# Optimization experiments

Measured on AMD Instinct MI355X. Metric: run time of the kernel, lower is better.

The kernel has to match this reference:

```python
import jax, jax.numpy as jnp
import numpy as np

NT, NC = 100000, 25000
ETT, ECT = 800000, 400000
DIN_T, DIN_C = 64, 32
H, C = 4, 32
HID = H * C  # 128
SLOPE = 0.2  # GATConv LeakyReLU negative slope


def setup_inputs() -> dict:
    key = jax.random.key(0)
    ks = jax.random.split(key, 24)
    def p(i, shape, s=0.05):
        return jax.random.normal(ks[i], shape, dtype=jnp.float32) * s
    return {
        'x_target': jax.random.normal(ks[0], (NT, DIN_T), dtype=jnp.float32),
        'x_context': jax.random.normal(ks[1], (NC, DIN_C), dtype=jnp.float32),
        'edge_tt': jax.random.randint(ks[2], (2, ETT), 0, NT),
        'edge_ct_src': jax.random.randint(ks[3], (ECT,), 0, NC),
        'edge_ct_dst': jax.random.randint(ks[4], (ECT,), 0, NT),
        'W_pre_t': p(5, (DIN_T, HID)), 'b_pre_t': jnp.zeros((HID,), jnp.float32),
        'W_pre_c': p(6, (DIN_C, HID)), 'b_pre_c': jnp.zeros((HID,), jnp.float32),
        'W_sd': p(7, (HID, HID)), 'att_src_sd': p(8, (H, C)), 'att_dst_sd': p(9, (H, C)), 'b_sd': jnp.zeros((HID,), jnp.float32),
        'W_ds': p(10, (HID, HID)), 'att_src_ds': p(11, (H, C)), 'att_dst_ds': p(12, (H, C)), 'b_ds': jnp.zeros((HID,), jnp.float32),
        'W_ct_src': p(13, (HID, HID)), 'W_ct_dst': p(14, (HID, HID)), 'att_src_ct': p(15, (H, C)), 'att_dst_ct': p(16, (H, C)), 'b_ct': jnp.zeros((HID,), jnp.float32),
        'W_out': p(17, (HID, HID)), 'b_out': jnp.zeros((HID,), jnp.float32),
    }


def _gat(h_src, h_dst, att_s, att_d, src, dst, n_dst, bias):
    # h_src: [N_src,H,C] transformed src feats; h_dst: [N_dst,H,C]
    a_s = jnp.einsum('nhc,hc->nh', h_src, att_s)  # [N_src,H]
    a_d = jnp.einsum('nhc,hc->nh', h_dst, att_d)  # [N_dst,H]
    e = a_s[src] + a_d[dst]                        # [E,H]
    e = jnp.where(e > 0, e, SLOPE * e)             # LeakyReLU(0.2)
    m = jax.ops.segment_max(e, dst, num_segments=n_dst)  # stable softmax per dst
    ex = jnp.exp(e - m[dst])
    den = jax.ops.segment_sum(ex, dst, num_segments=n_dst)
    alpha = ex / den[dst]                          # [E,H]
    msg = h_src[src] * alpha[:, :, None]           # [E,H,C]
    out = jax.ops.segment_sum(msg, dst, num_segments=n_dst)
    return out.reshape(n_dst, H * C) + bias


def reference(x_target, x_context, edge_tt, edge_ct_src, edge_ct_dst,
              W_pre_t, b_pre_t, W_pre_c, b_pre_c,
              W_sd, att_src_sd, att_dst_sd, b_sd,
              W_ds, att_src_ds, att_dst_ds, b_ds,
              W_ct_src, W_ct_dst, att_src_ct, att_dst_ct, b_ct,
              W_out, b_out):
    # HeteroDictLinear pretransform + relu
    h_t = jax.nn.relu(x_target @ W_pre_t + b_pre_t)   # [NT,128]
    h_c = jax.nn.relu(x_context @ W_pre_c + b_pre_c)  # [NC,128]
    res = h_t
    # DirGATConv on (target,to,target): forward + reversed, each w/ self-loops
    loops = jnp.arange(NT)
    src_f = jnp.concatenate([edge_tt[0], loops]); dst_f = jnp.concatenate([edge_tt[1], loops])
    src_r = jnp.concatenate([edge_tt[1], loops]); dst_r = jnp.concatenate([edge_tt[0], loops])
    hs = (h_t @ W_sd).reshape(NT, H, C)
    out_sd = _gat(hs, hs, att_src_sd, att_dst_sd, src_f, dst_f, NT, b_sd)
    hd = (h_t @ W_ds).reshape(NT, H, C)
    out_ds = _gat(hd, hd, att_src_ds, att_dst_ds, src_r, dst_r, NT, b_ds)
    out_tt = 0.5 * out_sd + 0.5 * out_ds  # (1-alpha), alpha with alpha=0.5
    # bipartite GATConv on (context,to,target), no self loops
    hcs = (h_c @ W_ct_src).reshape(NC, H, C)
    htd = (h_t @ W_ct_dst).reshape(NT, H, C)
    out_ct = _gat(hcs, htd, att_src_ct, att_dst_ct, edge_ct_src, edge_ct_dst, NT, b_ct)
    # HeteroConv aggr='mean' over the two edge types hitting 'target'
    x = 0.5 * (out_tt + out_ct)
    x = jax.nn.relu(x + res)  # skip connection + relu
    return x @ W_out + b_out
```

## Files before the change

kernel.cpp:

```cpp
#include <hip/hip_runtime.h>
#include <cstdint>
#include <cstddef>

typedef unsigned short u16;
typedef unsigned int u32;

#define NT 100000
#define NC 25000
#define ETT 800000
#define ECT 400000
#define SLOPE 0.2f
#define LOG2E 1.4426950408889634f
#define OFFS (NT + 4)

#define NBK 782
#define NBLK 256
#define CHT ((ETT + NBLK - 1) / NBLK)
#define CHC ((ECT + NBLK - 1) / NBLK)
#define TOTC (3 * NBK * NBLK)
#define NSB ((TOTC + 2047) / 2048)

typedef __attribute__((ext_vector_type(8))) short bf16x8;
typedef __attribute__((ext_vector_type(4))) float f32x4;

__device__ __forceinline__ u16 f2bf(float f) {
  u32 u = __float_as_uint(f);
  u32 r = (u >> 16) & 1u;
  return (u16)((u + 0x7fffu + r) >> 16);
}
__device__ __forceinline__ float lof(u32 p) { return __uint_as_float(p << 16); }
__device__ __forceinline__ float hif(u32 p) { return __uint_as_float(p & 0xffff0000u); }

#define GT_BLK ((NT + 31) / 32)
#define GC_BLK ((NC + 31) / 32)

__global__ __launch_bounds__(256) void transform_kernel(
    const float* __restrict__ Wsd, const float* __restrict__ AsSd, const float* __restrict__ AdSd,
    const float* __restrict__ Wds, const float* __restrict__ AsDs, const float* __restrict__ AdDs,
    const float* __restrict__ Wout,
    u16* __restrict__ bf_sd, u16* __restrict__ bf_ds, u16* __restrict__ bf_out,
    const float* __restrict__ Wcd, const float* __restrict__ attD,
    const float* __restrict__ bsd, const float* __restrict__ bds, const float* __restrict__ bct,
    float* __restrict__ cbias,
    const float* __restrict__ x_t, const float* __restrict__ Wpt, const float* __restrict__ bpt,
    u16* __restrict__ h_t, float* __restrict__ aD,
    const float* __restrict__ x_c, const float* __restrict__ Wpc, const float* __restrict__ bpc,
    const float* __restrict__ Wcs, const float* __restrict__ attS,
    u16* __restrict__ hc_bf, float* __restrict__ aS_c)
{
  __shared__ float s_a[32][33];
  __shared__ float s_b[32][128];
  __shared__ float s_c[32][132];
  const int b = blockIdx.x;
  const int t = threadIdx.x;

  if (b < 4) {
    if (b == 3) {
      if (t < 128) cbias[t] = 0.25f * bsd[t] + 0.25f * bds[t] + 0.5f * bct[t];
      return;
    }
    float* fS = &s_c[0][0];
    float* fD = fS + 512;
    const float* W = (b == 0) ? Wsd : (b == 1) ? Wds : Wout;
    const float* As = (b == 0) ? AsSd : AsDs;
    const float* Ad = (b == 0) ? AdSd : AdDs;
    u16* out = (b == 0) ? bf_sd : (b == 1) ? bf_ds : bf_out;
    const int tiles = (b == 2) ? 8 : 9;
    if (b < 2) {
      if (t < 128) {
        for (int h = 0; h < 4; ++h) {
          float s1 = 0.f, s2 = 0.f;
          for (int c = 0; c < 32; ++c) {
            const float wv = W[t * 128 + h * 32 + c];
            s1 = fmaf(wv, As[h * 32 + c], s1);
            s2 = fmaf(wv, Ad[h * 32 + c], s2);
          }
          fS[t * 4 + h] = s1 * LOG2E; fD[t * 4 + h] = s2 * LOG2E;
        }
      }
      __syncthreads();
    }
    const int total = tiles * 4 * 64 * 8;
    for (int i = t; i < total; i += 256) {
      const int j = i & 7, lane = (i >> 3) & 63, ks = (i >> 9) & 3, ti = i >> 11;
      const int k = ks * 32 + (lane >> 4) * 8 + j;
      const int n = ti * 16 + (lane & 15);
      float v;
      if (n < 128) v = W[k * 128 + n];
      else if (n < 132) v = fS[k * 4 + (n - 128)];
      else if (n < 136) v = fD[k * 4 + (n - 132)];
      else v = 0.f;
      out[i] = f2bf(v);
    }
    return;
  }

  if (b < 4 + GT_BLK) {
    float* s_fold = &s_c[0][0];
    if (t < 128) {
      for (int h = 0; h < 4; ++h) {
        float s = 0.f;
        for (int c = 0; c < 32; ++c)
          s = fmaf(Wcd[t * 128 + h * 32 + c], attD[h * 32 + c], s);
        s_fold[t * 4 + h] = s * LOG2E;
      }
    }
    const int row0 = (b - 4) * 32;
    const int rl = t >> 3, cg = t & 7;
    const int gr = row0 + rl;
    float acc[4][4];
    for (int g = 0; g < 4; ++g)
      for (int j = 0; j < 4; ++j)
        acc[g][j] = bpt[g * 32 + cg * 4 + j];
    for (int kc = 0; kc < 64; kc += 32) {
      {
        float4 f = make_float4(0.f, 0.f, 0.f, 0.f);
        if (gr < NT) f = *(const float4*)(x_t + (size_t)gr * 64 + kc + cg * 4);
        s_a[rl][cg * 4 + 0] = f.x; s_a[rl][cg * 4 + 1] = f.y;
        s_a[rl][cg * 4 + 2] = f.z; s_a[rl][cg * 4 + 3] = f.w;
      }
      for (int j = 0; j < 4; ++j) {
        const int idx = t + j * 256;
        const int k = idx >> 5, c4 = (idx & 31) * 4;
        *(float4*)&s_b[k][c4] = *(const float4*)(Wpt + (size_t)(kc + k) * 128 + c4);
      }
      __syncthreads();
#pragma unroll 8
      for (int k = 0; k < 32; ++k) {
        const float a = s_a[rl][k];
        for (int g = 0; g < 4; ++g) {
          const float4 w = *(const float4*)&s_b[k][g * 32 + cg * 4];
          acc[g][0] = fmaf(a, w.x, acc[g][0]);
          acc[g][1] = fmaf(a, w.y, acc[g][1]);
          acc[g][2] = fmaf(a, w.z, acc[g][2]);
          acc[g][3] = fmaf(a, w.w, acc[g][3]);
        }
      }
      __syncthreads();
    }
    if (gr < NT) {
      float p0 = 0.f, p1 = 0.f, p2 = 0.f, p3 = 0.f;
      for (int g = 0; g < 4; ++g) {
        for (int j = 0; j < 4; ++j) acc[g][j] = fmaxf(acc[g][j], 0.f);
        uint2 pk;
        pk.x = (u32)f2bf(acc[g][0]) | ((u32)f2bf(acc[g][1]) << 16);
        pk.y = (u32)f2bf(acc[g][2]) | ((u32)f2bf(acc[g][3]) << 16);
        *(uint2*)(h_t + (size_t)gr * 128 + g * 32 + cg * 4) = pk;
        for (int j = 0; j < 4; ++j) {
          const int col = g * 32 + cg * 4 + j;
          const float4 f4 = *(const float4*)&s_fold[col * 4];
          const float a = acc[g][j];
          p0 = fmaf(a, f4.x, p0); p1 = fmaf(a, f4.y, p1);
          p2 = fmaf(a, f4.z, p2); p3 = fmaf(a, f4.w, p3);
        }
      }
      for (int m = 1; m < 8; m <<= 1) {
        p0 += __shfl_xor(p0, m); p1 += __shfl_xor(p1, m);
        p2 += __shfl_xor(p2, m); p3 += __shfl_xor(p3, m);
      }
      if (cg == 0) *(float4*)(aD + (size_t)gr * 4) = make_float4(p0, p1, p2, p3);
    }
    return;
  }

  {
    const int row0 = (b - 4 - GT_BLK) * 32;
    const int rl = t >> 3, cg = t & 7;
    const int gr = row0 + rl;
    {
      float4 f = make_float4(0.f, 0.f, 0.f, 0.f);
      if (gr < NC) f = *(const float4*)(x_c + (size_t)gr * 32 + cg * 4);
      s_a[rl][cg * 4 + 0] = f.x; s_a[rl][cg * 4 + 1] = f.y;
      s_a[rl][cg * 4 + 2] = f.z; s_a[rl][cg * 4 + 3] = f.w;
    }
    for (int j = 0; j < 4; ++j) {
      const int idx = t + j * 256;
      const int k = idx >> 5, c4 = (idx & 31) * 4;
      *(float4*)&s_b[k][c4] = *(const float4*)(Wpc + (size_t)k * 128 + c4);
    }
    __syncthreads();
    float acc[4][4];
    for (int g = 0; g < 4; ++g)
      for (int j = 0; j < 4; ++j) acc[g][j] = bpc[g * 32 + cg * 4 + j];
#pragma unroll 8
    for (int k = 0; k < 32; ++k) {
      const float a = s_a[rl][k];
      for (int g = 0; g < 4; ++g) {
        const float4 w = *(const float4*)&s_b[k][g * 32 + cg * 4];
        acc[g][0] = fmaf(a, w.x, acc[g][0]);
        acc[g][1] = fmaf(a, w.y, acc[g][1]);
        acc[g][2] = fmaf(a, w.z, acc[g][2]);
        acc[g][3] = fmaf(a, w.w, acc[g][3]);
      }
    }
    for (int g = 0; g < 4; ++g)
      *(float4*)&s_c[rl][g * 32 + cg * 4] =
          make_float4(fmaxf(acc[g][0], 0.f), fmaxf(acc[g][1], 0.f),
                      fmaxf(acc[g][2], 0.f), fmaxf(acc[g][3], 0.f));
    __syncthreads();
    float acc2[4][4];
    for (int g = 0; g < 4; ++g)
      for (int j = 0; j < 4; ++j) acc2[g][j] = 0.f;
    for (int kc = 0; kc < 128; kc += 32) {
      for (int j = 0; j < 4; ++j) {
        const int idx = t + j * 256;
        const int k = idx >> 5, c4 = (idx & 31) * 4;
        *(float4*)&s_b[k][c4] = *(const float4*)(Wcs + (size_t)(kc + k) * 128 + c4);
      }
      __syncthreads();
#pragma unroll 8
      for (int k = 0; k < 32; ++k) {
        const float a = s_c[rl][kc + k];
        for (int g = 0; g < 4; ++g) {
          const float4 w = *(const float4*)&s_b[k][g * 32 + cg * 4];
          acc2[g][0] = fmaf(a, w.x, acc2[g][0]);
          acc2[g][1] = fmaf(a, w.y, acc2[g][1]);
          acc2[g][2] = fmaf(a, w.z, acc2[g][2]);
          acc2[g][3] = fmaf(a, w.w, acc2[g][3]);
        }
      }
      __syncthreads();
    }
    if (gr < NC) {
      float pS[4];
      for (int g = 0; g < 4; ++g) {
        uint2 pk;
        pk.x = (u32)f2bf(acc2[g][0]) | ((u32)f2bf(acc2[g][1]) << 16);
        pk.y = (u32)f2bf(acc2[g][2]) | ((u32)f2bf(acc2[g][3]) << 16);
        *(uint2*)(hc_bf + (size_t)gr * 128 + g * 32 + cg * 4) = pk;
        const float4 as4 = *(const float4*)(attS + g * 32 + cg * 4);
        pS[g] = acc2[g][0] * as4.x + acc2[g][1] * as4.y + acc2[g][2] * as4.z + acc2[g][3] * as4.w;
      }
      for (int m = 1; m < 8; m <<= 1)
        for (int g = 0; g < 4; ++g) pS[g] += __shfl_xor(pS[g], m);
      if (cg == 0)
        *(float4*)(aS_c + (size_t)gr * 4) =
            make_float4(pS[0] * LOG2E, pS[1] * LOG2E, pS[2] * LOG2E, pS[3] * LOG2E);
    }
  }
}

__global__ __launch_bounds__(256) void mfma_logits2_kernel(
    const short* __restrict__ A, const short* __restrict__ Bsd, const short* __restrict__ Bds,
    u16* __restrict__ hs, float* __restrict__ aSsd, float* __restrict__ aDsd,
    u16* __restrict__ hd, float* __restrict__ aSds, float* __restrict__ aDds, int M)
{
  __shared__ __align__(16) float lds[4][16][148];
  const int wv = threadIdx.x >> 6, lane = threadIdx.x & 63;
  const int quad = lane >> 4, l16 = lane & 15;
  const int row0 = blockIdx.x * 64 + wv * 16;
  const int arow = min(row0 + l16, M - 1);
  const short* ap = A + (size_t)arow * 128 + quad * 8;
  bf16x8 af[4];
  for (int ks = 0; ks < 4; ++ks) af[ks] = *(const bf16x8*)(ap + ks * 32);
  const int row = row0 + l16;
  const int idx = lane & 7, rr = lane >> 3;
  for (int pass = 0; pass < 2; ++pass) {
    const short* B = pass ? Bds : Bsd;
    u16* outb = pass ? hd : hs;
    float* aS = pass ? aSds : aSsd;
    float* aD = pass ? aDds : aDsd;
    f32x4 acc[9];
    for (int t = 0; t < 9; ++t) acc[t] = (f32x4){0.f, 0.f, 0.f, 0.f};
    for (int ks = 0; ks < 4; ++ks)
      for (int t = 0; t < 9; ++t) {
        const bf16x8 bf = *(const bf16x8*)(B + ((t * 4 + ks) * 64 + lane) * 8);
        acc[t] = __builtin_amdgcn_mfma_f32_16x16x32_bf16(af[ks], bf, acc[t], 0, 0, 0);
      }
    for (int t = 0; t < 9; ++t)
      for (int r = 0; r < 4; ++r)
        lds[wv][quad * 4 + r][t * 16 + l16] = acc[t][r];
    __syncthreads();
    if (row < M) {
      for (int g = 0; g < 8; ++g) {
        const f32x4 v = *(const f32x4*)&lds[wv][l16][g * 16 + quad * 4];
        uint2 pk;
        pk.x = (u32)f2bf(v[0]) | ((u32)f2bf(v[1]) << 16);
        pk.y = (u32)f2bf(v[2]) | ((u32)f2bf(v[3]) << 16);
        *(uint2*)(outb + (size_t)row * 128 + g * 16 + quad * 4) = pk;
      }
    }
    for (int p = 0; p < 2; ++p) {
      const int lr = p * 8 + rr;
      const int n = row0 + lr;
      if (n < M) {
        const float v = lds[wv][lr][128 + idx];
        if (idx < 4) aS[(size_t)n * 4 + idx] = v;
        else aD[(size_t)n * 4 + idx - 4] = v;
      }
    }
    __syncthreads();
  }
}

__global__ __launch_bounds__(256) void mfma_out_kernel(
    const short* __restrict__ A, const short* __restrict__ B,
    const float* __restrict__ bias, float* __restrict__ out, int M)
{
  __shared__ __align__(16) float lds[4][16][132];
  const int wv = threadIdx.x >> 6, lane = threadIdx.x & 63;
  const int quad = lane >> 4, l16 = lane & 15;
  const int row0 = blockIdx.x * 64 + wv * 16;
  const int arow = min(row0 + l16, M - 1);
  const short* ap = A + (size_t)arow * 128 + quad * 8;
  bf16x8 af[4];
  for (int ks = 0; ks < 4; ++ks) af[ks] = *(const bf16x8*)(ap + ks * 32);
  f32x4 acc[8];
  for (int t = 0; t < 8; ++t) acc[t] = (f32x4){0.f, 0.f, 0.f, 0.f};
  for (int ks = 0; ks < 4; ++ks)
    for (int t = 0; t < 8; ++t) {
      const bf16x8 bf = *(const bf16x8*)(B + ((t * 4 + ks) * 64 + lane) * 8);
      acc[t] = __builtin_amdgcn_mfma_f32_16x16x32_bf16(af[ks], bf, acc[t], 0, 0, 0);
    }
  for (int t = 0; t < 8; ++t)
    for (int r = 0; r < 4; ++r)
      lds[wv][quad * 4 + r][t * 16 + l16] = acc[t][r];
  __syncthreads();
  const int row = row0 + l16;
  if (row < M) {
    for (int g = 0; g < 8; ++g) {
      const int col = g * 16 + quad * 4;
      f32x4 v = *(const f32x4*)&lds[wv][l16][col];
      const f32x4 b4 = *(const f32x4*)(bias + col);
      v = v + b4;
      *(f32x4*)(out + (size_t)row * 128 + col) = v;
    }
  }
}

__global__ __launch_bounds__(256) void hist_blk_kernel(const int* __restrict__ tt_src,
    const int* __restrict__ tt_dst, const int* __restrict__ ect_d, int* __restrict__ cntblk)
{
  __shared__ int h[3 * NBK];
  const int t = threadIdx.x, b = blockIdx.x;
  for (int i = t; i < 3 * NBK; i += 256) h[i] = 0;
  __syncthreads();
  const int lo = b * CHT, hi = min(lo + CHT, ETT);
  for (int i = lo + t; i < hi; i += 256) {
    atomicAdd(&h[tt_dst[i] >> 7], 1);
    atomicAdd(&h[NBK + (tt_src[i] >> 7)], 1);
  }
  const int lo2 = b * CHC, hi2 = min(lo2 + CHC, ECT);
  for (int i = lo2 + t; i < hi2; i += 256)
    atomicAdd(&h[2 * NBK + (ect_d[i] >> 7)], 1);
  __syncthreads();
  for (int i = t; i < 3 * NBK; i += 256)
    cntblk[(size_t)i * NBLK + b] = h[i];
}

__global__ __launch_bounds__(256) void scan2_blk_kernel(const int* __restrict__ in,
    int* __restrict__ out, int* __restrict__ bsum)
{
  const int t = threadIdx.x, b = blockIdx.x;
  const int idx = b * 2048 + t * 8;
  int v[8];
  int s = 0;
  if (idx < TOTC) {
    const int4 q0 = *(const int4*)(in + idx);
    const int4 q1 = *(const int4*)(in + idx + 4);
    int x;
    x = q0.x; v[0] = s; s += x;  x = q0.y; v[1] = s; s += x;
    x = q0.z; v[2] = s; s += x;  x = q0.w; v[3] = s; s += x;
    x = q1.x; v[4] = s; s += x;  x = q1.y; v[5] = s; s += x;
    x = q1.z; v[6] = s; s += x;  x = q1.w; v[7] = s; s += x;
  } else {
    for (int j = 0; j < 8; ++j) v[j] = 0;
  }
  __shared__ int sh[256];
  sh[t] = s;
  __syncthreads();
  for (int d = 1; d < 256; d <<= 1) {
    const int u = (t >= d) ? sh[t - d] : 0;
    __syncthreads();
    sh[t] += u;
    __syncthreads();
  }
  const int excl = (t == 0) ? 0 : sh[t - 1];
  if (idx < TOTC) {
    int4 q0, q1;
    q0.x = excl + v[0]; q0.y = excl + v[1]; q0.z = excl + v[2]; q0.w = excl + v[3];
    q1.x = excl + v[4]; q1.y = excl + v[5]; q1.z = excl + v[6]; q1.w = excl + v[7];
    *(int4*)(out + idx) = q0;
    *(int4*)(out + idx + 4) = q1;
  }
  if (t == 255) bsum[b] = sh[255];
}

__global__ __launch_bounds__(512) void scan2_top_kernel(const int* __restrict__ bsum,
    int* __restrict__ bpre)
{
  __shared__ int sh[512];
  const int t = threadIdx.x;
  const int orig = (t < NSB) ? bsum[t] : 0;
  sh[t] = orig;
  __syncthreads();
  for (int d = 1; d < 512; d <<= 1) {
    const int v = (t >= d) ? sh[t - d] : 0;
    __syncthreads();
    sh[t] += v;
    __syncthreads();
  }
  if (t < NSB) bpre[t] = sh[t] - orig;
}

__global__ __launch_bounds__(256) void bin_kernel(const int* __restrict__ tt_src,
    const int* __restrict__ tt_dst, const int* __restrict__ ect_s, const int* __restrict__ ect_d,
    const int* __restrict__ scanned, const int* __restrict__ bpre, u32* __restrict__ bin)
{
  __shared__ int cur[3 * NBK];
  const int t = threadIdx.x, b = blockIdx.x;
  for (int i = t; i < 3 * NBK; i += 256) {
    const int idx = i * NBLK + b;
    cur[i] = scanned[idx] + bpre[idx >> 11];
  }
  __syncthreads();
  const int lo = b * CHT, hi = min(lo + CHT, ETT);
  for (int i = lo + t; i < hi; i += 256) {
    const int s = tt_src[i], d = tt_dst[i];
    int p = atomicAdd(&cur[d >> 7], 1);
    bin[p] = ((u32)(d & 127) << 17) | (u32)s;
    p = atomicAdd(&cur[NBK + (s >> 7)], 1);
    bin[p] = ((u32)(s & 127) << 17) | (u32)d;
  }
  const int lo2 = b * CHC, hi2 = min(lo2 + CHC, ECT);
  for (int i = lo2 + t; i < hi2; i += 256) {
    const int s = ect_s[i], d = ect_d[i];
    const int p = atomicAdd(&cur[2 * NBK + (d >> 7)], 1);
    bin[p] = ((u32)(d & 127) << 17) | (u32)s;
  }
}

__global__ __launch_bounds__(256) void bucket_fill_kernel(const int* __restrict__ scanned,
    const int* __restrict__ bpre, const u32* __restrict__ bin,
    int* __restrict__ offs, int* __restrict__ big_el)
{
  const int rel = blockIdx.x / NBK;
  const int bucket = blockIdx.x - rel * NBK;
  const int t = threadIdx.x;
  __shared__ int s_cnt[128], s_exc[128], s_cur[128];
  if (t < 128) s_cnt[t] = 0;
  __syncthreads();
  const int bi = blockIdx.x * NBLK;
  const int base = scanned[bi] + bpre[bi >> 11];
  const int nxt = (blockIdx.x == 3 * NBK - 1) ? (2 * ETT + ECT)
                                              : scanned[bi + NBLK] + bpre[(bi + NBLK) >> 11];
  const int size = nxt - base;
  for (int i = t; i < size; i += 256)
    atomicAdd(&s_cnt[bin[base + i] >> 17], 1);
  __syncthreads();
  if (t < 128) s_exc[t] = s_cnt[t];
  __syncthreads();
  for (int d = 1; d < 128; d <<= 1) {
    int v = 0;
    if (t < 128 && t >= d) v = s_exc[t - d];
    __syncthreads();
    if (t < 128) s_exc[t] += v;
    __syncthreads();
  }
  const int relbase = rel * ETT;
  const int obase = base - relbase;
  int* off_rel = offs + (size_t)rel * OFFS;
  const int node0 = bucket * 128;
  if (t < 128) {
    const int excl = s_exc[t] - s_cnt[t];
    s_cur[t] = obase + excl;
    if (node0 + t < NT) off_rel[node0 + t] = obase + excl;
  }
  if (t == 0 && bucket == NBK - 1) off_rel[NT] = obase + size;
  __syncthreads();
  int* el_rel = big_el + relbase;
  for (int i = t; i < size; i += 256) {
    const u32 e = bin[base + i];
    const int pos = atomicAdd(&s_cur[e >> 17], 1);
    el_rel[pos] = (int)(e & 0x1FFFFu);
  }
}

__device__ __forceinline__ void gat_pipe16(const int* __restrict__ off,
    const int* __restrict__ el, const float* __restrict__ aS, const float* __restrict__ aD,
    const u16* __restrict__ hb, int d, int h, int cb, int self_loop, float w,
    float* __restrict__ acc)
{
  const float ad = aD[(size_t)d * 4 + h];
  const int beg = off[d];
  const int m = off[d + 1] - beg;
  const int cnt = m + self_loop;
  if (cnt <= 0) return;
  float den = 0.f;
  float a0 = 0.f, a1 = 0.f, a2 = 0.f, a3 = 0.f, a4 = 0.f, a5 = 0.f, a6 = 0.f, a7 = 0.f;
  int sB = (1 < m) ? el[beg + 1] : d;
  {
    const int sA0 = (0 < m) ? el[beg] : d;
    float eA = aS[(size_t)sA0 * 4 + h];
    uint4 pA = *(const uint4*)(hb + (size_t)sA0 * 128 + cb);
    for (int k = 0; k < cnt; ++k) {
      const int sC = (k + 2 < m) ? el[beg + k + 2] : d;
      const float eB = aS[(size_t)sB * 4 + h];
      const uint4 pB = *(const uint4*)(hb + (size_t)sB * 128 + cb);
      float ea = eA + ad;
      ea = ea > 0.f ? ea : SLOPE * ea;
      const float ex = exp2f(ea);
      den += ex;
      a0 = fmaf(ex, lof(pA.x), a0); a1 = fmaf(ex, hif(pA.x), a1);
      a2 = fmaf(ex, lof(pA.y), a2); a3 = fmaf(ex, hif(pA.y), a3);
      a4 = fmaf(ex, lof(pA.z), a4); a5 = fmaf(ex, hif(pA.z), a5);
      a6 = fmaf(ex, lof(pA.w), a6); a7 = fmaf(ex, hif(pA.w), a7);
      eA = eB; pA = pB; sB = sC;
    }
  }
  const float s = w / den;
  acc[0] = fmaf(a0, s, acc[0]); acc[1] = fmaf(a1, s, acc[1]);
  acc[2] = fmaf(a2, s, acc[2]); acc[3] = fmaf(a3, s, acc[3]);
  acc[4] = fmaf(a4, s, acc[4]); acc[5] = fmaf(a5, s, acc[5]);
  acc[6] = fmaf(a6, s, acc[6]); acc[7] = fmaf(a7, s, acc[7]);
}

__global__ __launch_bounds__(256) void gather_all_kernel(
    const int* __restrict__ off_f, const int* __restrict__ el_f,
    const float* __restrict__ aS_sd, const float* __restrict__ aD_sd, const u16* __restrict__ hs,
    const int* __restrict__ off_r, const int* __restrict__ el_r,
    const float* __restrict__ aS_ds, const float* __restrict__ aD_ds, const u16* __restrict__ hd,
    const int* __restrict__ off_c, const int* __restrict__ el_c,
    const float* __restrict__ aS_ct, const float* __restrict__ aD_ct, const u16* __restrict__ hc,
    const u16* __restrict__ skip, const float* __restrict__ cbias, u16* __restrict__ x)
{
  const int d = blockIdx.x * 16 + (threadIdx.x >> 4);
  if (d >= NT) return;
  const int lg = threadIdx.x & 15;
  const int h = lg >> 2;
  const int cb = lg * 8;
  float acc[8];
  for (int i = 0; i < 8; ++i) acc[i] = 0.f;
  gat_pipe16(off_f, el_f, aS_sd, aD_sd, hs, d, h, cb, 1, 0.25f, acc);
  gat_pipe16(off_r, el_r, aS_ds, aD_ds, hd, d, h, cb, 1, 0.25f, acc);
  gat_pipe16(off_c, el_c, aS_ct, aD_ct, hc, d, h, cb, 0, 0.5f, acc);
  const uint4 sk = *(const uint4*)(skip + (size_t)d * 128 + cb);
  const float4 cb0 = *(const float4*)(cbias + cb);
  const float4 cb1 = *(const float4*)(cbias + cb + 4);
  const float o0 = fmaxf(acc[0] + cb0.x + lof(sk.x), 0.f);
  const float o1 = fmaxf(acc[1] + cb0.y + hif(sk.x), 0.f);
  const float o2 = fmaxf(acc[2] + cb0.z + lof(sk.y), 0.f);
  const float o3 = fmaxf(acc[3] + cb0.w + hif(sk.y), 0.f);
  const float o4 = fmaxf(acc[4] + cb1.x + lof(sk.z), 0.f);
  const float o5 = fmaxf(acc[5] + cb1.y + hif(sk.z), 0.f);
  const float o6 = fmaxf(acc[6] + cb1.z + lof(sk.w), 0.f);
  const float o7 = fmaxf(acc[7] + cb1.w + hif(sk.w), 0.f);
  uint4 r;
  r.x = (u32)f2bf(o0) | ((u32)f2bf(o1) << 16);
  r.y = (u32)f2bf(o2) | ((u32)f2bf(o3) << 16);
  r.z = (u32)f2bf(o4) | ((u32)f2bf(o5) << 16);
  r.w = (u32)f2bf(o6) | ((u32)f2bf(o7) << 16);
  *(uint4*)(x + (size_t)d * 128 + cb) = r;
}

extern "C" void kernel_launch(void* const* d_in, const int* in_sizes, int n_in,
                              void* d_out, int out_size, void* d_ws, size_t ws_size,
                              hipStream_t stream)
{
  const float* x_t   = (const float*)d_in[0];
  const float* x_c   = (const float*)d_in[1];
  const int*   e_tt  = (const int*)d_in[2];
  const int*   ect_s = (const int*)d_in[3];
  const int*   ect_d = (const int*)d_in[4];
  const float* Wpt = (const float*)d_in[5];   const float* bpt = (const float*)d_in[6];
  const float* Wpc = (const float*)d_in[7];   const float* bpc = (const float*)d_in[8];
  const float* Wsd = (const float*)d_in[9];   const float* As_sd = (const float*)d_in[10];
  const float* Ad_sd = (const float*)d_in[11]; const float* bsd = (const float*)d_in[12];
  const float* Wds = (const float*)d_in[13];  const float* As_ds = (const float*)d_in[14];
  const float* Ad_ds = (const float*)d_in[15]; const float* bds = (const float*)d_in[16];
  const float* Wcs = (const float*)d_in[17];  const float* Wcd = (const float*)d_in[18];
  const float* As_ct = (const float*)d_in[19]; const float* Ad_ct = (const float*)d_in[20];
  const float* bct = (const float*)d_in[21];
  const float* Wout = (const float*)d_in[22]; const float* bout = (const float*)d_in[23];

  char* p = (char*)d_ws;
  size_t off = 0;
  auto alloc = [&](size_t bytes) { char* r = p + off; off += (bytes + 255) & ~(size_t)255; return r; };
  u16* ht_bf   = (u16*)alloc((size_t)NT * 128 * 2);
  u16* hs_bf   = (u16*)alloc((size_t)NT * 128 * 2);
  u16* hd_bf   = (u16*)alloc((size_t)NT * 128 * 2);
  u16* hc_bf   = (u16*)alloc((size_t)NC * 128 * 2);
  u16* x_bf    = (u16*)alloc((size_t)NT * 128 * 2);
  float* aS_sd = (float*)alloc((size_t)NT * 4 * 4);
  float* aD_sd = (float*)alloc((size_t)NT * 4 * 4);
  float* aS_ds = (float*)alloc((size_t)NT * 4 * 4);
  float* aD_ds = (float*)alloc((size_t)NT * 4 * 4);
  float* aS_ct = (float*)alloc((size_t)NC * 4 * 4);
  float* aD_ct = (float*)alloc((size_t)NT * 4 * 4);
  int* cntblk  = (int*)alloc((size_t)TOTC * 4);
  int* scanned = (int*)alloc((size_t)TOTC * 4);
  u32* bin     = (u32*)alloc((size_t)(2 * ETT + ECT) * 4);
  int* big_el  = (int*)alloc((size_t)(2 * ETT + ECT) * 4);
  int* offs    = (int*)alloc((size_t)3 * OFFS * 4);
  int* bsum    = (int*)alloc((size_t)NSB * 4);
  int* bpre    = (int*)alloc((size_t)NSB * 4);
  float* cbias   = (float*)alloc(128 * 4);
  u16* bfrag_sd  = (u16*)alloc((size_t)9 * 4 * 64 * 8 * 2);
  u16* bfrag_ds  = (u16*)alloc((size_t)9 * 4 * 64 * 8 * 2);
  u16* bfrag_out = (u16*)alloc((size_t)8 * 4 * 64 * 8 * 2);

  int* off_f = offs;
  int* off_r = offs + OFFS;
  int* off_c = offs + 2 * OFFS;
  int* el_f = big_el;
  int* el_r = big_el + ETT;
  int* el_c = big_el + 2 * ETT;

  const int* tt_src = e_tt;
  const int* tt_dst = e_tt + ETT;

  const int gM = (NT + 63) / 64;

  hist_blk_kernel<<<NBLK, 256, 0, stream>>>(tt_src, tt_dst, ect_d, cntblk);
  scan2_blk_kernel<<<NSB, 256, 0, stream>>>(cntblk, scanned, bsum);
  scan2_top_kernel<<<1, 512, 0, stream>>>(bsum, bpre);
  bin_kernel<<<NBLK, 256, 0, stream>>>(tt_src, tt_dst, ect_s, ect_d, scanned, bpre, bin);
  bucket_fill_kernel<<<3 * NBK, 256, 0, stream>>>(scanned, bpre, bin, offs, big_el);

  transform_kernel<<<4 + GT_BLK + GC_BLK, 256, 0, stream>>>(
      Wsd, As_sd, Ad_sd, Wds, As_ds, Ad_ds, Wout,
      bfrag_sd, bfrag_ds, bfrag_out,
      Wcd, Ad_ct, bsd, bds, bct, cbias,
      x_t, Wpt, bpt, ht_bf, aD_ct,
      x_c, Wpc, bpc, Wcs, As_ct, hc_bf, aS_ct);

  mfma_logits2_kernel<<<gM, 256, 0, stream>>>((const short*)ht_bf,
      (const short*)bfrag_sd, (const short*)bfrag_ds,
      hs_bf, aS_sd, aD_sd, hd_bf, aS_ds, aD_ds, NT);

  gather_all_kernel<<<(NT + 15) / 16, 256, 0, stream>>>(
      off_f, el_f, aS_sd, aD_sd, hs_bf,
      off_r, el_r, aS_ds, aD_ds, hd_bf,
      off_c, el_c, aS_ct, aD_ct, hc_bf,
      ht_bf, cbias, x_bf);

  mfma_out_kernel<<<gM, 256, 0, stream>>>((const short*)x_bf, (const short*)bfrag_out,
                                          bout, (float*)d_out, NT);
}
```

Baseline: 428.4 us.

## Fuse CSR build stages into transform and logits kernels, drop top-level scan

Merges the histogram kernel into the transform kernel and the binning kernel into the logits MFMA kernel by giving each fused launch extra leading blocks, so the independent graph-building and dense work run concurrently. The separate top-level scan launch is removed: each consumer block recomputes the block-sum prefix in shared memory, and the scan tile grows to 4096 elements so one 256-thread pass covers it. Bucket fill now stages the sorted edge list in LDS and writes it out coalesced when the bucket fits. This cuts kernel launches and scattered global writes, at the cost of redundant prefix computation per block and higher LDS use.

```diff
diff --git a/kernel.cpp b/kernel.cpp
--- a/kernel.cpp
+++ b/kernel.cpp
@@ -18,7 +18,11 @@
 #define CHT ((ETT + NBLK - 1) / NBLK)
 #define CHC ((ECT + NBLK - 1) / NBLK)
 #define TOTC (3 * NBK * NBLK)
-#define NSB ((TOTC + 2047) / 2048)
+#define NSB ((TOTC + 4095) / 4096)
+#define FILL_CAP 4096
+
+#define GT_BLK ((NT + 31) / 32)
+#define GC_BLK ((NC + 31) / 32)
 
 typedef __attribute__((ext_vector_type(8))) short bf16x8;
 typedef __attribute__((ext_vector_type(4))) float f32x4;
@@ -31,10 +35,26 @@
 __device__ __forceinline__ float lof(u32 p) { return __uint_as_float(p << 16); }
 __device__ __forceinline__ float hif(u32 p) { return __uint_as_float(p & 0xffff0000u); }
 
-#define GT_BLK ((NT + 31) / 32)
-#define GC_BLK ((NC + 31) / 32)
-
-__global__ __launch_bounds__(256) void transform_kernel(
+__device__ __forceinline__ void compute_bpre(const int* __restrict__ bsum, int* s_bpre) {
+  const int t = threadIdx.x;
+  const int v = (t < NSB) ? bsum[t] : 0;
+  s_bpre[t] = v;
+  __syncthreads();
+  for (int d = 1; d < 256; d <<= 1) {
+    const int u = (t >= d) ? s_bpre[t - d] : 0;
+    __syncthreads();
+    s_bpre[t] += u;
+    __syncthreads();
+  }
+  const int incl = s_bpre[t];
+  __syncthreads();
+  s_bpre[t] = incl - v;
+  __syncthreads();
+}
+
+__global__ __launch_bounds__(256) void transform_hist_kernel(
+    const int* __restrict__ tt_src, const int* __restrict__ tt_dst,
+    const int* __restrict__ ect_d, int* __restrict__ cntblk,
     const float* __restrict__ Wsd, const float* __restrict__ AsSd, const float* __restrict__ AdSd,
     const float* __restrict__ Wds, const float* __restrict__ AsDs, const float* __restrict__ AdDs,
     const float* __restrict__ Wout,
@@ -51,8 +71,28 @@
   __shared__ float s_a[32][33];
   __shared__ float s_b[32][128];
   __shared__ float s_c[32][132];
-  const int b = blockIdx.x;
   const int t = threadIdx.x;
+
+  if (blockIdx.x < NBLK) {
+    int* h = (int*)&s_b[0][0];
+    const int b = blockIdx.x;
+    for (int i = t; i < 3 * NBK; i += 256) h[i] = 0;
+    __syncthreads();
+    const int lo = b * CHT, hi = min(lo + CHT, ETT);
+    for (int i = lo + t; i < hi; i += 256) {
+      atomicAdd(&h[tt_dst[i] >> 7], 1);
+      atomicAdd(&h[NBK + (tt_src[i] >> 7)], 1);
+    }
+    const int lo2 = b * CHC, hi2 = min(lo2 + CHC, ECT);
+    for (int i = lo2 + t; i < hi2; i += 256)
+      atomicAdd(&h[2 * NBK + (ect_d[i] >> 7)], 1);
+    __syncthreads();
+    for (int i = t; i < 3 * NBK; i += 256)
+      cntblk[(size_t)i * NBLK + b] = h[i];
+    return;
+  }
+
+  const int b = blockIdx.x - NBLK;
 
   if (b < 4) {
     if (b == 3) {
@@ -240,15 +280,90 @@
   }
 }
 
-__global__ __launch_bounds__(256) void mfma_logits2_kernel(
+__global__ __launch_bounds__(256) void scan2_blk_kernel(const int* __restrict__ in,
+    int* __restrict__ out, int* __restrict__ bsum)
+{
+  const int t = threadIdx.x, b = blockIdx.x;
+  const int idx = b * 4096 + t * 16;
+  int v[16];
+  int s = 0;
+  if (idx < TOTC) {
+#pragma unroll
+    for (int q = 0; q < 4; ++q) {
+      const int4 qq = *(const int4*)(in + idx + q * 4);
+      v[q * 4 + 0] = s; s += qq.x;
+      v[q * 4 + 1] = s; s += qq.y;
+      v[q * 4 + 2] = s; s += qq.z;
+      v[q * 4 + 3] = s; s += qq.w;
+    }
+  } else {
+    for (int j = 0; j < 16; ++j) v[j] = 0;
+  }
+  __shared__ int sh[256];
+  sh[t] = s;
+  __syncthreads();
+  for (int d = 1; d < 256; d <<= 1) {
+    const int u = (t >= d) ? sh[t - d] : 0;
+    __syncthreads();
+    sh[t] += u;
+    __syncthreads();
+  }
+  const int excl = (t == 0) ? 0 : sh[t - 1];
+  if (idx < TOTC) {
+#pragma unroll
+    for (int q = 0; q < 4; ++q) {
+      int4 qo;
+      qo.x = excl + v[q * 4 + 0]; qo.y = excl + v[q * 4 + 1];
+      qo.z = excl + v[q * 4 + 2]; qo.w = excl + v[q * 4 + 3];
+      *(int4*)(out + idx + q * 4) = qo;
+    }
+  }
+  if (t == 255) bsum[b] = sh[255];
+}
+
+__global__ __launch_bounds__(256) void bin_logits2_kernel(
+    const int* __restrict__ tt_src, const int* __restrict__ tt_dst,
+    const int* __restrict__ ect_s, const int* __restrict__ ect_d,
+    const int* __restrict__ scanned, const int* __restrict__ bsum, u32* __restrict__ bin,
     const short* __restrict__ A, const short* __restrict__ Bsd, const short* __restrict__ Bds,
     u16* __restrict__ hs, float* __restrict__ aSsd, float* __restrict__ aDsd,
     u16* __restrict__ hd, float* __restrict__ aSds, float* __restrict__ aDds, int M)
 {
-  __shared__ __align__(16) float lds[4][16][148];
-  const int wv = threadIdx.x >> 6, lane = threadIdx.x & 63;
+  __shared__ __align__(16) float ldsf[4][16][148];
+  const int t = threadIdx.x;
+
+  if (blockIdx.x < NBLK) {
+    int* cur = (int*)&ldsf[0][0][0];
+    int* s_bpre = cur + 3 * NBK;
+    compute_bpre(bsum, s_bpre);
+    const int b = blockIdx.x;
+    for (int i = t; i < 3 * NBK; i += 256) {
+      const int idx = i * NBLK + b;
+      cur[i] = scanned[idx] + s_bpre[idx >> 12];
+    }
+    __syncthreads();
+    const int lo = b * CHT, hi = min(lo + CHT, ETT);
+    for (int i = lo + t; i < hi; i += 256) {
+      const int s = tt_src[i], d = tt_dst[i];
+      int p = atomicAdd(&cur[d >> 7], 1);
+      bin[p] = ((u32)(d & 127) << 17) | (u32)s;
+      p = atomicAdd(&cur[NBK + (s >> 7)], 1);
+      bin[p] = ((u32)(s & 127) << 17) | (u32)d;
+    }
+    const int lo2 = b * CHC, hi2 = min(lo2 + CHC, ECT);
+    for (int i = lo2 + t; i < hi2; i += 256) {
+      const int s = ect_s[i], d = ect_d[i];
+      const int p = atomicAdd(&cur[2 * NBK + (d >> 7)], 1);
+      bin[p] = ((u32)(d & 127) << 17) | (u32)s;
+    }
+    return;
+  }
+
+  float (*lds)[16][148] = ldsf;
+  const int blk = blockIdx.x - NBLK;
+  const int wv = t >> 6, lane = t & 63;
   const int quad = lane >> 4, l16 = lane & 15;
-  const int row0 = blockIdx.x * 64 + wv * 16;
+  const int row0 = blk * 64 + wv * 16;
   const int arow = min(row0 + l16, M - 1);
   const short* ap = A + (size_t)arow * 128 + quad * 8;
   bf16x8 af[4];
@@ -261,15 +376,15 @@
     float* aS = pass ? aSds : aSsd;
     float* aD = pass ? aDds : aDsd;
     f32x4 acc[9];
-    for (int t = 0; t < 9; ++t) acc[t] = (f32x4){0.f, 0.f, 0.f, 0.f};
+    for (int ti = 0; ti < 9; ++ti) acc[ti] = (f32x4){0.f, 0.f, 0.f, 0.f};
     for (int ks = 0; ks < 4; ++ks)
-      for (int t = 0; t < 9; ++t) {
-        const bf16x8 bf = *(const bf16x8*)(B + ((t * 4 + ks) * 64 + lane) * 8);
-        acc[t] = __builtin_amdgcn_mfma_f32_16x16x32_bf16(af[ks], bf, acc[t], 0, 0, 0);
-      }
-    for (int t = 0; t < 9; ++t)
+      for (int ti = 0; ti < 9; ++ti) {
+        const bf16x8 bf = *(const bf16x8*)(B + ((ti * 4 + ks) * 64 + lane) * 8);
+        acc[ti] = __builtin_amdgcn_mfma_f32_16x16x32_bf16(af[ks], bf, acc[ti], 0, 0, 0);
+      }
+    for (int ti = 0; ti < 9; ++ti)
       for (int r = 0; r < 4; ++r)
-        lds[wv][quad * 4 + r][t * 16 + l16] = acc[t][r];
+        lds[wv][quad * 4 + r][ti * 16 + l16] = acc[ti][r];
     __syncthreads();
     if (row < M) {
       for (int g = 0; g < 8; ++g) {
@@ -290,6 +405,66 @@
       }
     }
     __syncthreads();
+  }
+}
+
+__global__ __launch_bounds__(256) void bucket_fill_kernel(const int* __restrict__ scanned,
+    const int* __restrict__ bsum, const u32* __restrict__ bin,
+    int* __restrict__ offs, int* __restrict__ big_el)
+{
+  __shared__ int s_cnt[128], s_exc[128], s_cur[128], s_bpre[256];
+  __shared__ int s_el[FILL_CAP];
+  const int t = threadIdx.x;
+  compute_bpre(bsum, s_bpre);
+  const int rel = blockIdx.x / NBK;
+  const int bucket = blockIdx.x - rel * NBK;
+  if (t < 128) s_cnt[t] = 0;
+  const int bi = blockIdx.x * NBLK;
+  const int base = scanned[bi] + s_bpre[bi >> 12];
+  const int nxt = (blockIdx.x == 3 * NBK - 1)
+                      ? (2 * ETT + ECT)
+                      : scanned[bi + NBLK] + s_bpre[(bi + NBLK) >> 12];
+  __syncthreads();
+  const int size = nxt - base;
+  for (int i = t; i < size; i += 256)
+    atomicAdd(&s_cnt[bin[base + i] >> 17], 1);
+  __syncthreads();
+  if (t < 128) s_exc[t] = s_cnt[t];
+  __syncthreads();
+  for (int d = 1; d < 128; d <<= 1) {
+    int v = 0;
+    if (t < 128 && t >= d) v = s_exc[t - d];
+    __syncthreads();
+    if (t < 128) s_exc[t] += v;
+    __syncthreads();
+  }
+  const int relbase = rel * ETT;
+  const int obase = base - relbase;
+  int* off_rel = offs + (size_t)rel * OFFS;
+  const int node0 = bucket * 128;
+  if (t < 128) {
+    const int excl = s_exc[t] - s_cnt[t];
+    s_cur[t] = excl;
+    if (node0 + t < NT) off_rel[node0 + t] = obase + excl;
+  }
+  if (t == 0 && bucket == NBK - 1) off_rel[NT] = obase + size;
+  __syncthreads();
+  int* el_rel = big_el + relbase;
+  if (size <= FILL_CAP) {
+    for (int i = t; i < size; i += 256) {
+      const u32 e = bin[base + i];
+      const int pos = atomicAdd(&s_cur[e >> 17], 1);
+      s_el[pos] = (int)(e & 0x1FFFFu);
+    }
+    __syncthreads();
+    for (int i = t; i < size; i += 256)
+      el_rel[obase + i] = s_el[i];
+  } else {
+    for (int i = t; i < size; i += 256) {
+      const u32 e = bin[base + i];
+      const int pos = atomicAdd(&s_cur[e >> 17], 1);
+      el_rel[obase + pos] = (int)(e & 0x1FFFFu);
+    }
   }
 }
 
@@ -325,154 +500,6 @@
       v = v + b4;
       *(f32x4*)(out + (size_t)row * 128 + col) = v;
     }
-  }
-}
-
-__global__ __launch_bounds__(256) void hist_blk_kernel(const int* __restrict__ tt_src,
-    const int* __restrict__ tt_dst, const int* __restrict__ ect_d, int* __restrict__ cntblk)
-{
-  __shared__ int h[3 * NBK];
-  const int t = threadIdx.x, b = blockIdx.x;
-  for (int i = t; i < 3 * NBK; i += 256) h[i] = 0;
-  __syncthreads();
-  const int lo = b * CHT, hi = min(lo + CHT, ETT);
-  for (int i = lo + t; i < hi; i += 256) {
-    atomicAdd(&h[tt_dst[i] >> 7], 1);
-    atomicAdd(&h[NBK + (tt_src[i] >> 7)], 1);
-  }
-  const int lo2 = b * CHC, hi2 = min(lo2 + CHC, ECT);
-  for (int i = lo2 + t; i < hi2; i += 256)
-    atomicAdd(&h[2 * NBK + (ect_d[i] >> 7)], 1);
-  __syncthreads();
-  for (int i = t; i < 3 * NBK; i += 256)
-    cntblk[(size_t)i * NBLK + b] = h[i];
-}
-
-__global__ __launch_bounds__(256) void scan2_blk_kernel(const int* __restrict__ in,
-    int* __restrict__ out, int* __restrict__ bsum)
-{
-  const int t = threadIdx.x, b = blockIdx.x;
-  const int idx = b * 2048 + t * 8;
-  int v[8];
-  int s = 0;
-  if (idx < TOTC) {
-    const int4 q0 = *(const int4*)(in + idx);
-    const int4 q1 = *(const int4*)(in + idx + 4);
-    int x;
-    x = q0.x; v[0] = s; s += x;  x = q0.y; v[1] = s; s += x;
-    x = q0.z; v[2] = s; s += x;  x = q0.w; v[3] = s; s += x;
-    x = q1.x; v[4] = s; s += x;  x = q1.y; v[5] = s; s += x;
-    x = q1.z; v[6] = s; s += x;  x = q1.w; v[7] = s; s += x;
-  } else {
-    for (int j = 0; j < 8; ++j) v[j] = 0;
-  }
-  __shared__ int sh[256];
-  sh[t] = s;
-  __syncthreads();
-  for (int d = 1; d < 256; d <<= 1) {
-    const int u = (t >= d) ? sh[t - d] : 0;
-    __syncthreads();
-    sh[t] += u;
-    __syncthreads();
-  }
-  const int excl = (t == 0) ? 0 : sh[t - 1];
-  if (idx < TOTC) {
-    int4 q0, q1;
-    q0.x = excl + v[0]; q0.y = excl + v[1]; q0.z = excl + v[2]; q0.w = excl + v[3];
-    q1.x = excl + v[4]; q1.y = excl + v[5]; q1.z = excl + v[6]; q1.w = excl + v[7];
-    *(int4*)(out + idx) = q0;
-    *(int4*)(out + idx + 4) = q1;
-  }
-  if (t == 255) bsum[b] = sh[255];
-}
-
-__global__ __launch_bounds__(512) void scan2_top_kernel(const int* __restrict__ bsum,
-    int* __restrict__ bpre)
-{
-  __shared__ int sh[512];
-  const int t = threadIdx.x;
-  const int orig = (t < NSB) ? bsum[t] : 0;
-  sh[t] = orig;
-  __syncthreads();
-  for (int d = 1; d < 512; d <<= 1) {
-    const int v = (t >= d) ? sh[t - d] : 0;
-    __syncthreads();
-    sh[t] += v;
-    __syncthreads();
-  }
-  if (t < NSB) bpre[t] = sh[t] - orig;
-}
-
-__global__ __launch_bounds__(256) void bin_kernel(const int* __restrict__ tt_src,
-    const int* __restrict__ tt_dst, const int* __restrict__ ect_s, const int* __restrict__ ect_d,
-    const int* __restrict__ scanned, const int* __restrict__ bpre, u32* __restrict__ bin)
-{
-  __shared__ int cur[3 * NBK];
-  const int t = threadIdx.x, b = blockIdx.x;
-  for (int i = t; i < 3 * NBK; i += 256) {
-    const int idx = i * NBLK + b;
-    cur[i] = scanned[idx] + bpre[idx >> 11];
-  }
-  __syncthreads();
-  const int lo = b * CHT, hi = min(lo + CHT, ETT);
-  for (int i = lo + t; i < hi; i += 256) {
-    const int s = tt_src[i], d = tt_dst[i];
-    int p = atomicAdd(&cur[d >> 7], 1);
-    bin[p] = ((u32)(d & 127) << 17) | (u32)s;
-    p = atomicAdd(&cur[NBK + (s >> 7)], 1);
-    bin[p] = ((u32)(s & 127) << 17) | (u32)d;
-  }
-  const int lo2 = b * CHC, hi2 = min(lo2 + CHC, ECT);
-  for (int i = lo2 + t; i < hi2; i += 256) {
-    const int s = ect_s[i], d = ect_d[i];
-    const int p = atomicAdd(&cur[2 * NBK + (d >> 7)], 1);
-    bin[p] = ((u32)(d & 127) << 17) | (u32)s;
-  }
-}
-
-__global__ __launch_bounds__(256) void bucket_fill_kernel(const int* __restrict__ scanned,
-    const int* __restrict__ bpre, const u32* __restrict__ bin,
-    int* __restrict__ offs, int* __restrict__ big_el)
-{
-  const int rel = blockIdx.x / NBK;
-  const int bucket = blockIdx.x - rel * NBK;
-  const int t = threadIdx.x;
-  __shared__ int s_cnt[128], s_exc[128], s_cur[128];
-  if (t < 128) s_cnt[t] = 0;
-  __syncthreads();
-  const int bi = blockIdx.x * NBLK;
-  const int base = scanned[bi] + bpre[bi >> 11];
-  const int nxt = (blockIdx.x == 3 * NBK - 1) ? (2 * ETT + ECT)
-                                              : scanned[bi + NBLK] + bpre[(bi + NBLK) >> 11];
-  const int size = nxt - base;
-  for (int i = t; i < size; i += 256)
-    atomicAdd(&s_cnt[bin[base + i] >> 17], 1);
-  __syncthreads();
-  if (t < 128) s_exc[t] = s_cnt[t];
-  __syncthreads();
-  for (int d = 1; d < 128; d <<= 1) {
-    int v = 0;
-    if (t < 128 && t >= d) v = s_exc[t - d];
-    __syncthreads();
-    if (t < 128) s_exc[t] += v;
-    __syncthreads();
-  }
-  const int relbase = rel * ETT;
-  const int obase = base - relbase;
-  int* off_rel = offs + (size_t)rel * OFFS;
-  const int node0 = bucket * 128;
-  if (t < 128) {
-    const int excl = s_exc[t] - s_cnt[t];
-    s_cur[t] = obase + excl;
-    if (node0 + t < NT) off_rel[node0 + t] = obase + excl;
-  }
-  if (t == 0 && bucket == NBK - 1) off_rel[NT] = obase + size;
-  __syncthreads();
-  int* el_rel = big_el + relbase;
-  for (int i = t; i < size; i += 256) {
-    const u32 e = bin[base + i];
-    const int pos = atomicAdd(&s_cur[e >> 17], 1);
-    el_rel[pos] = (int)(e & 0x1FFFFu);
   }
 }
 
@@ -593,7 +620,6 @@
   int* big_el  = (int*)alloc((size_t)(2 * ETT + ECT) * 4);
   int* offs    = (int*)alloc((size_t)3 * OFFS * 4);
   int* bsum    = (int*)alloc((size_t)NSB * 4);
-  int* bpre    = (int*)alloc((size_t)NSB * 4);
   float* cbias   = (float*)alloc(128 * 4);
   u16* bfrag_sd  = (u16*)alloc((size_t)9 * 4 * 64 * 8 * 2);
   u16* bfrag_ds  = (u16*)alloc((size_t)9 * 4 * 64 * 8 * 2);
@@ -611,22 +637,22 @@
 
   const int gM = (NT + 63) / 64;
 
-  hist_blk_kernel<<<NBLK, 256, 0, stream>>>(tt_src, tt_dst, ect_d, cntblk);
-  scan2_blk_kernel<<<NSB, 256, 0, stream>>>(cntblk, scanned, bsum);
-  scan2_top_kernel<<<1, 512, 0, stream>>>(bsum, bpre);
-  bin_kernel<<<NBLK, 256, 0, stream>>>(tt_src, tt_dst, ect_s, ect_d, scanned, bpre, bin);
-  bucket_fill_kernel<<<3 * NBK, 256, 0, stream>>>(scanned, bpre, bin, offs, big_el);
-
-  transform_kernel<<<4 + GT_BLK + GC_BLK, 256, 0, stream>>>(
+  transform_hist_kernel<<<NBLK + 4 + GT_BLK + GC_BLK, 256, 0, stream>>>(
+      tt_src, tt_dst, ect_d, cntblk,
       Wsd, As_sd, Ad_sd, Wds, As_ds, Ad_ds, Wout,
       bfrag_sd, bfrag_ds, bfrag_out,
       Wcd, Ad_ct, bsd, bds, bct, cbias,
       x_t, Wpt, bpt, ht_bf, aD_ct,
       x_c, Wpc, bpc, Wcs, As_ct, hc_bf, aS_ct);
 
-  mfma_logits2_kernel<<<gM, 256, 0, stream>>>((const short*)ht_bf,
-      (const short*)bfrag_sd, (const short*)bfrag_ds,
+  scan2_blk_kernel<<<NSB, 256, 0, stream>>>(cntblk, scanned, bsum);
+
+  bin_logits2_kernel<<<NBLK + gM, 256, 0, stream>>>(
+      tt_src, tt_dst, ect_s, ect_d, scanned, bsum, bin,
+      (const short*)ht_bf, (const short*)bfrag_sd, (const short*)bfrag_ds,
       hs_bf, aS_sd, aD_sd, hd_bf, aS_ds, aD_ds, NT);
+
+  bucket_fill_kernel<<<3 * NBK, 256, 0, stream>>>(scanned, bsum, bin, offs, big_el);
 
   gather_all_kernel<<<(NT + 15) / 16, 256, 0, stream>>>(
       off_f, el_f, aS_sd, aD_sd, hs_bf,
```

Measured after the change: 411.7 us. 1.04x faster.
